# Kernel optimization log

Measured on AMD Instinct MI355X. Metric: run time of the kernel, lower is better.

The kernel has to match this reference:

```python
import jax, jax.numpy as jnp
import numpy as np

N, F, D, H = 8192, 128, 128, 2
LEAKY_ALPHA = 0.3  # keras.layers.LeakyReLU default


def setup_inputs() -> dict:
    key = jax.random.key(0)
    ks = jax.random.split(key, 8)
    x = jax.random.normal(ks[0], (N, F), dtype=jnp.float32)
    # sparse-ish binary adjacency with self loops, stored dense (as the module does)
    adj = (jax.random.uniform(ks[1], (N, N)) < 0.01).astype(jnp.float32)
    adj = jnp.clip(adj + jnp.eye(N, dtype=jnp.float32), 0.0, 1.0)
    s = 1.0 / np.sqrt(F)
    Wmap = jax.random.normal(ks[2], (H, F, D), dtype=jnp.float32) * s
    a1_w = jax.random.normal(ks[3], (H, D), dtype=jnp.float32) * (1.0 / np.sqrt(D))
    a2_w = jax.random.normal(ks[4], (H, D), dtype=jnp.float32) * (1.0 / np.sqrt(D))
    a1_b = jnp.zeros((H,), dtype=jnp.float32)
    a2_b = jnp.zeros((H,), dtype=jnp.float32)
    kernel = jax.random.normal(ks[5], (H, F, D), dtype=jnp.float32) * s
    bias = jnp.zeros((H, N, D), dtype=jnp.float32)
    return {"x": x, "adj": adj, "Wmap": Wmap, "a1_w": a1_w, "a1_b": a1_b,
            "a2_w": a2_w, "a2_b": a2_b, "kernel": kernel, "bias": bias}


def reference(x, adj, Wmap, a1_w, a1_b, a2_w, a2_b, kernel, bias):
    # per-head Conv1D(k=1, no bias): node-wise linear map  [H, N, D]
    mapped = jnp.einsum('nf,hfd->hnd', x, Wmap)
    # per-head Conv1D(k=1) scalar scores  [H, N]
    sa1 = jnp.einsum('hnd,hd->hn', mapped, a1_w) + a1_b[:, None]
    sa2 = jnp.einsum('hnd,hd->hn', mapped, a2_w) + a2_b[:, None]
    # additive score masked multiplicatively by adjacency:  [H, N, N]
    w = adj[None, :, :] * sa1[:, :, None] + adj[None, :, :] * sa2[:, None, :]
    w = jnp.where(w >= 0, w, LEAKY_ALPHA * w)
    att = jax.nn.softmax(w, axis=-1)  # softmax over neighbors (incl. zeroed entries, as in source)
    value = jnp.einsum('nf,hfd->hnd', x, kernel)
    out = jnp.einsum('hnm,hmd->hnd', att, value) + bias  # [H, N, D]
    return out.mean(axis=0)  # attn_heads_reduction='average', linear activation
```

## Files before the change

kernel.cpp:

```cpp
#include <hip/hip_runtime.h>

#define NN 8192
#define FF 128
#define DD 128
#define HH 2
#define ALPHA 0.3f
#define MAXNNZ 1024

typedef float v4f __attribute__((ext_vector_type(4)));

__global__ __launch_bounds__(256) void prep_kernel(
    const float* __restrict__ Wmap, const float* __restrict__ a1w,
    const float* __restrict__ a2w, const float* __restrict__ x,
    float* __restrict__ c1, float* __restrict__ c2, float* __restrict__ xsum) {
  int b = blockIdx.x;
  int t = threadIdx.x;
  if (b == 128) {
    int h = t >> 7, f = t & 127;
    const float* wrow = Wmap + ((size_t)h * FF + f) * DD;
    const float* a1 = a1w + h * DD;
    const float* a2 = a2w + h * DD;
    float s1 = 0.f, s2 = 0.f;
    #pragma unroll 8
    for (int d = 0; d < DD; d++) {
      float w = wrow[d];
      s1 += w * a1[d];
      s2 += w * a2[d];
    }
    c1[t] = s1;
    c2[t] = s2;
  } else {
    int f = t & 127, rh = t >> 7;
    const float* xp = x + ((size_t)(b * 64 + rh) * FF) + f;
    float s = 0.f;
    #pragma unroll 8
    for (int r = 0; r < 64; r += 2) s += xp[(size_t)r * FF];
    atomicAdd(&xsum[f], s);
  }
}

__global__ __launch_bounds__(128) void sa_kernel(
    const float* __restrict__ x, const float* __restrict__ c1,
    const float* __restrict__ c2, const float* __restrict__ a1b,
    const float* __restrict__ a2b, float* __restrict__ sa1, float* __restrict__ sa2) {
  int n = blockIdx.x;
  int f = threadIdx.x;
  float xv = x[(size_t)n * FF + f];
  float p00 = xv * c1[f];
  float p01 = xv * c1[FF + f];
  float p10 = xv * c2[f];
  float p11 = xv * c2[FF + f];
  #pragma unroll
  for (int o = 32; o > 0; o >>= 1) {
    p00 += __shfl_down(p00, o);
    p01 += __shfl_down(p01, o);
    p10 += __shfl_down(p10, o);
    p11 += __shfl_down(p11, o);
  }
  __shared__ float part[2][4];
  int w = f >> 6;
  if ((f & 63) == 0) {
    part[w][0] = p00; part[w][1] = p01; part[w][2] = p10; part[w][3] = p11;
  }
  __syncthreads();
  if (f == 0) {
    sa1[n]      = part[0][0] + part[1][0] + a1b[0];
    sa1[NN + n] = part[0][1] + part[1][1] + a1b[1];
    sa2[n]      = part[0][2] + part[1][2] + a2b[0];
    sa2[NN + n] = part[0][3] + part[1][3] + a2b[1];
  }
}

__global__ __launch_bounds__(128) void colsum_kernel(
    const float* __restrict__ xsum, const float* __restrict__ kern,
    float* __restrict__ colsum) {
  int h = blockIdx.x, d = threadIdx.x;
  const float* kb = kern + (size_t)h * FF * DD + d;
  float s = 0.f;
  #pragma unroll 8
  for (int f = 0; f < FF; f++) s += xsum[f] * kb[(size_t)f * DD];
  colsum[h * DD + d] = s;
}

__global__ __launch_bounds__(256) void gat_gather(
    const float* __restrict__ adj, const float* __restrict__ x,
    const float* __restrict__ sa1, const float* __restrict__ sa2,
    float* __restrict__ gs, float* __restrict__ cinv) {
  int i = blockIdx.x;
  __shared__ int idxbuf[MAXNNZ];
  __shared__ float em1buf[HH][MAXNNZ];
  __shared__ int cnt;
  __shared__ float wred[4][HH];
  __shared__ float sume_sh[HH];
  __shared__ float red2[HH][FF];
  int t = threadIdx.x;
  if (t == 0) cnt = 0;
  __syncthreads();

  const v4f* arow = (const v4f*)(adj + (size_t)i * NN);
  #pragma unroll
  for (int q = 0; q < 8; q++) {
    int f4 = q * 256 + t;
    v4f a = __builtin_nontemporal_load(&arow[f4]);
    int j0 = f4 * 4;
    if (a.x != 0.f) { int p = atomicAdd(&cnt, 1); if (p < MAXNNZ) idxbuf[p] = j0; }
    if (a.y != 0.f) { int p = atomicAdd(&cnt, 1); if (p < MAXNNZ) idxbuf[p] = j0 + 1; }
    if (a.z != 0.f) { int p = atomicAdd(&cnt, 1); if (p < MAXNNZ) idxbuf[p] = j0 + 2; }
    if (a.w != 0.f) { int p = atomicAdd(&cnt, 1); if (p < MAXNNZ) idxbuf[p] = j0 + 3; }
  }
  __syncthreads();
  int count = min(cnt, MAXNNZ);

  float s10 = sa1[i];
  float s11 = sa1[NN + i];
  float l0 = 0.f, l1 = 0.f;
  for (int k = t; k < count; k += 256) {
    int j = idxbuf[k];
    float w0 = s10 + sa2[j];
    float w1 = s11 + sa2[NN + j];
    w0 = (w0 >= 0.f) ? w0 : ALPHA * w0;
    w1 = (w1 >= 0.f) ? w1 : ALPHA * w1;
    float e0 = __expf(w0) - 1.f;
    float e1 = __expf(w1) - 1.f;
    em1buf[0][k] = e0;
    em1buf[1][k] = e1;
    l0 += e0;
    l1 += e1;
  }
  #pragma unroll
  for (int o = 32; o > 0; o >>= 1) {
    l0 += __shfl_down(l0, o);
    l1 += __shfl_down(l1, o);
  }
  int wid = t >> 6;
  if ((t & 63) == 0) { wred[wid][0] = l0; wred[wid][1] = l1; }
  __syncthreads();
  if (t == 0) {
    sume_sh[0] = wred[0][0] + wred[1][0] + wred[2][0] + wred[3][0];
    sume_sh[1] = wred[0][1] + wred[1][1] + wred[2][1] + wred[3][1];
  }
  __syncthreads();

  int ks = t >> 7, f = t & 127;
  float a0 = 0.f, a1 = 0.f;
  const float* xb = x + f;
  #pragma unroll 4
  for (int k = ks; k < count; k += 2) {
    int j = idxbuf[k];
    float xv = xb[(size_t)j * FF];
    a0 += em1buf[0][k] * xv;
    a1 += em1buf[1][k] * xv;
  }
  if (ks == 1) { red2[0][f] = a0; red2[1][f] = a1; }
  __syncthreads();
  if (ks == 0) {
    float inv0 = 0.5f / ((float)NN + sume_sh[0]);
    float inv1 = 0.5f / ((float)NN + sume_sh[1]);
    float g0 = (a0 + red2[0][f]) * inv0;
    float g1 = (a1 + red2[1][f]) * inv1;
    gs[(size_t)i * (HH * FF) + f]      = g0;
    gs[(size_t)i * (HH * FF) + FF + f] = g1;
    if (f == 0) { cinv[i] = inv0; cinv[NN + i] = inv1; }
  }
}

__global__ __launch_bounds__(256) void out_gemm(
    const float* __restrict__ gs, const float* __restrict__ kern,
    const float* __restrict__ cinv, const float* __restrict__ colsum,
    const float* __restrict__ bias, float* __restrict__ out) {
  int row0 = blockIdx.x * 32;
  __shared__ float Bl[64 * 128];
  __shared__ float Al[32 * 129];
  const float4* Bg4 = (const float4*)kern;
  const float4* Ag4 = (const float4*)(gs + (size_t)row0 * 256);
  float4* Bl4 = (float4*)Bl;
  int tid = threadIdx.x;
  int cg = tid & 31;
  int rg = tid >> 5;
  float4 acc[4];
  #pragma unroll
  for (int m = 0; m < 4; m++) acc[m] = make_float4(0.f, 0.f, 0.f, 0.f);

  for (int ka = 0; ka < 2; ka++) {
    __syncthreads();
    #pragma unroll
    for (int q = 0; q < 4; q++) {
      int idx = q * 256 + tid;
      int r = idx >> 5, c4 = idx & 31;
      float4 g = Ag4[r * 64 + ka * 32 + c4];
      Al[r * 129 + c4 * 4 + 0] = g.x;
      Al[r * 129 + c4 * 4 + 1] = g.y;
      Al[r * 129 + c4 * 4 + 2] = g.z;
      Al[r * 129 + c4 * 4 + 3] = g.w;
    }
    #pragma unroll
    for (int kpi = 0; kpi < 2; kpi++) {
      int kp = ka * 2 + kpi;
      __syncthreads();
      #pragma unroll
      for (int q = 0; q < 8; q++)
        Bl4[q * 256 + tid] = Bg4[kp * 2048 + q * 256 + tid];
      __syncthreads();
      for (int k2 = 0; k2 < 64; k2++) {
        float4 bv = *(const float4*)&Bl[k2 * 128 + cg * 4];
        #pragma unroll
        for (int m = 0; m < 4; m++) {
          float av = Al[(rg + m * 8) * 129 + kpi * 64 + k2];
          acc[m].x += av * bv.x;
          acc[m].y += av * bv.y;
          acc[m].z += av * bv.z;
          acc[m].w += av * bv.w;
        }
      }
    }
  }

  float4 cs0 = *(const float4*)&colsum[cg * 4];
  float4 cs1 = *(const float4*)&colsum[DD + cg * 4];
  #pragma unroll
  for (int m = 0; m < 4; m++) {
    int r = row0 + rg + m * 8;
    float ci0 = cinv[r];
    float ci1 = cinv[NN + r];
    float4 b0 = *(const float4*)&bias[((size_t)0 * NN + r) * DD + cg * 4];
    float4 b1 = *(const float4*)&bias[((size_t)1 * NN + r) * DD + cg * 4];
    float4 o;
    o.x = acc[m].x + ci0 * cs0.x + ci1 * cs1.x + 0.5f * (b0.x + b1.x);
    o.y = acc[m].y + ci0 * cs0.y + ci1 * cs1.y + 0.5f * (b0.y + b1.y);
    o.z = acc[m].z + ci0 * cs0.z + ci1 * cs1.z + 0.5f * (b0.z + b1.z);
    o.w = acc[m].w + ci0 * cs0.w + ci1 * cs1.w + 0.5f * (b0.w + b1.w);
    *(float4*)&out[(size_t)r * DD + cg * 4] = o;
  }
}

extern "C" void kernel_launch(void* const* d_in, const int* in_sizes, int n_in,
                              void* d_out, int out_size, void* d_ws, size_t ws_size,
                              hipStream_t stream) {
  const float* x    = (const float*)d_in[0];
  const float* adj  = (const float*)d_in[1];
  const float* Wmap = (const float*)d_in[2];
  const float* a1w  = (const float*)d_in[3];
  const float* a1b  = (const float*)d_in[4];
  const float* a2w  = (const float*)d_in[5];
  const float* a2b  = (const float*)d_in[6];
  const float* kern = (const float*)d_in[7];
  const float* bias = (const float*)d_in[8];
  float* out = (float*)d_out;
  float* ws  = (float*)d_ws;

  float* c1     = ws;
  float* c2     = ws + 256;
  float* sa1    = ws + 512;
  float* sa2    = ws + 16896;
  float* xsum   = ws + 33280;
  float* colsum = ws + 33408;
  float* cinv   = ws + 33664;
  float* gs     = ws + 50048;

  hipMemsetAsync(xsum, 0, FF * sizeof(float), stream);
  prep_kernel<<<129, 256, 0, stream>>>(Wmap, a1w, a2w, x, c1, c2, xsum);
  sa_kernel<<<NN, 128, 0, stream>>>(x, c1, c2, a1b, a2b, sa1, sa2);
  colsum_kernel<<<HH, 128, 0, stream>>>(xsum, kern, colsum);
  gat_gather<<<NN, 256, 0, stream>>>(adj, x, sa1, sa2, gs, cinv);
  out_gemm<<<NN / 32, 256, 0, stream>>>(gs, kern, cinv, colsum, bias, out);
}
```

Before: 428.6 us.

## Split adjacency scan from edge gather and fold colsum term into GEMM input

Splits the fused gather kernel into an adjacency scan that writes per-row neighbor index lists and a separate edge-gather kernel that vectorizes feature loads across 8 edge groups. The constant softmax term is folded in by adding xsum into the gathered row before the GEMM, removing the colsum kernel and the cinv epilogue. sa2 is packed as float2, and the GEMM uses float4 LDS reads with padded rows. This adds global traffic for the index lists and an extra launch.

```diff
diff --git a/kernel.cpp b/kernel.cpp
--- a/kernel.cpp
+++ b/kernel.cpp
@@ -42,7 +42,7 @@
 __global__ __launch_bounds__(128) void sa_kernel(
     const float* __restrict__ x, const float* __restrict__ c1,
     const float* __restrict__ c2, const float* __restrict__ a1b,
-    const float* __restrict__ a2b, float* __restrict__ sa1, float* __restrict__ sa2) {
+    const float* __restrict__ a2b, float* __restrict__ sa1, float* __restrict__ sa2p) {
   int n = blockIdx.x;
   int f = threadIdx.x;
   float xv = x[(size_t)n * FF + f];
@@ -66,37 +66,20 @@
   if (f == 0) {
     sa1[n]      = part[0][0] + part[1][0] + a1b[0];
     sa1[NN + n] = part[0][1] + part[1][1] + a1b[1];
-    sa2[n]      = part[0][2] + part[1][2] + a2b[0];
-    sa2[NN + n] = part[0][3] + part[1][3] + a2b[1];
-  }
-}
-
-__global__ __launch_bounds__(128) void colsum_kernel(
-    const float* __restrict__ xsum, const float* __restrict__ kern,
-    float* __restrict__ colsum) {
-  int h = blockIdx.x, d = threadIdx.x;
-  const float* kb = kern + (size_t)h * FF * DD + d;
-  float s = 0.f;
-  #pragma unroll 8
-  for (int f = 0; f < FF; f++) s += xsum[f] * kb[(size_t)f * DD];
-  colsum[h * DD + d] = s;
-}
-
-__global__ __launch_bounds__(256) void gat_gather(
-    const float* __restrict__ adj, const float* __restrict__ x,
-    const float* __restrict__ sa1, const float* __restrict__ sa2,
-    float* __restrict__ gs, float* __restrict__ cinv) {
+    ((float2*)sa2p)[n] = make_float2(part[0][2] + part[1][2] + a2b[0],
+                                     part[0][3] + part[1][3] + a2b[1]);
+  }
+}
+
+__global__ __launch_bounds__(256) void adj_scan(
+    const float* __restrict__ adj, int* __restrict__ counts,
+    int* __restrict__ idxw) {
   int i = blockIdx.x;
   __shared__ int idxbuf[MAXNNZ];
-  __shared__ float em1buf[HH][MAXNNZ];
   __shared__ int cnt;
-  __shared__ float wred[4][HH];
-  __shared__ float sume_sh[HH];
-  __shared__ float red2[HH][FF];
   int t = threadIdx.x;
   if (t == 0) cnt = 0;
   __syncthreads();
-
   const v4f* arow = (const v4f*)(adj + (size_t)i * NN);
   #pragma unroll
   for (int q = 0; q < 8; q++) {
@@ -110,14 +93,36 @@
   }
   __syncthreads();
   int count = min(cnt, MAXNNZ);
+  if (t == 0) counts[i] = count;
+  int* dst = idxw + (size_t)i * MAXNNZ;
+  for (int k = t; k < count; k += 256) dst[k] = idxbuf[k];
+}
+
+__global__ __launch_bounds__(256) void edge_gather(
+    const int* __restrict__ counts, const int* __restrict__ idxw,
+    const float* __restrict__ x, const float* __restrict__ sa1,
+    const float* __restrict__ sa2p, const float* __restrict__ xsum,
+    float* __restrict__ gs) {
+  int i = blockIdx.x;
+  __shared__ int idxbuf[MAXNNZ];
+  __shared__ float em1buf[HH][MAXNNZ];
+  __shared__ float wred[4][HH];
+  __shared__ float sume_sh[HH];
+  __shared__ v4f vred[HH][8][32];
+  int t = threadIdx.x;
+  int count = counts[i];
+  const int* src = idxw + (size_t)i * MAXNNZ;
+  for (int k = t; k < count; k += 256) idxbuf[k] = src[k];
+  __syncthreads();
 
   float s10 = sa1[i];
   float s11 = sa1[NN + i];
   float l0 = 0.f, l1 = 0.f;
   for (int k = t; k < count; k += 256) {
     int j = idxbuf[k];
-    float w0 = s10 + sa2[j];
-    float w1 = s11 + sa2[NN + j];
+    float2 s2 = ((const float2*)sa2p)[j];
+    float w0 = s10 + s2.x;
+    float w1 = s11 + s2.y;
     w0 = (w0 >= 0.f) ? w0 : ALPHA * w0;
     w1 = (w1 >= 0.f) ? w1 : ALPHA * w1;
     float e0 = __expf(w0) - 1.f;
@@ -141,45 +146,47 @@
   }
   __syncthreads();
 
-  int ks = t >> 7, f = t & 127;
-  float a0 = 0.f, a1 = 0.f;
-  const float* xb = x + f;
+  int sub = t & 31;
+  int eg  = t >> 5;
+  v4f acc0 = {0.f, 0.f, 0.f, 0.f}, acc1 = {0.f, 0.f, 0.f, 0.f};
+  const v4f* xb = (const v4f*)x;
   #pragma unroll 4
-  for (int k = ks; k < count; k += 2) {
+  for (int k = eg; k < count; k += 8) {
     int j = idxbuf[k];
-    float xv = xb[(size_t)j * FF];
-    a0 += em1buf[0][k] * xv;
-    a1 += em1buf[1][k] * xv;
-  }
-  if (ks == 1) { red2[0][f] = a0; red2[1][f] = a1; }
-  __syncthreads();
-  if (ks == 0) {
-    float inv0 = 0.5f / ((float)NN + sume_sh[0]);
-    float inv1 = 0.5f / ((float)NN + sume_sh[1]);
-    float g0 = (a0 + red2[0][f]) * inv0;
-    float g1 = (a1 + red2[1][f]) * inv1;
-    gs[(size_t)i * (HH * FF) + f]      = g0;
-    gs[(size_t)i * (HH * FF) + FF + f] = g1;
-    if (f == 0) { cinv[i] = inv0; cinv[NN + i] = inv1; }
+    v4f xv = xb[(size_t)j * 32 + sub];
+    acc0 += em1buf[0][k] * xv;
+    acc1 += em1buf[1][k] * xv;
+  }
+  vred[0][eg][sub] = acc0;
+  vred[1][eg][sub] = acc1;
+  __syncthreads();
+  if (t < 64) {
+    int h = t >> 5, s = t & 31;
+    v4f v = vred[h][0][s];
+    #pragma unroll
+    for (int e = 1; e < 8; e++) v += vred[h][e][s];
+    float inv = 0.5f / ((float)NN + sume_sh[h]);
+    v4f xs = ((const v4f*)xsum)[s];
+    v4f g = (v + xs) * inv;
+    ((v4f*)(gs + (size_t)i * (HH * FF)))[h * 32 + s] = g;
   }
 }
 
 __global__ __launch_bounds__(256) void out_gemm(
     const float* __restrict__ gs, const float* __restrict__ kern,
-    const float* __restrict__ cinv, const float* __restrict__ colsum,
     const float* __restrict__ bias, float* __restrict__ out) {
   int row0 = blockIdx.x * 32;
   __shared__ float Bl[64 * 128];
-  __shared__ float Al[32 * 129];
+  __shared__ float Al[32 * 132];
   const float4* Bg4 = (const float4*)kern;
   const float4* Ag4 = (const float4*)(gs + (size_t)row0 * 256);
   float4* Bl4 = (float4*)Bl;
   int tid = threadIdx.x;
   int cg = tid & 31;
   int rg = tid >> 5;
-  float4 acc[4];
-  #pragma unroll
-  for (int m = 0; m < 4; m++) acc[m] = make_float4(0.f, 0.f, 0.f, 0.f);
+  v4f acc[4];
+  #pragma unroll
+  for (int m = 0; m < 4; m++) acc[m] = (v4f){0.f, 0.f, 0.f, 0.f};
 
   for (int ka = 0; ka < 2; ka++) {
     __syncthreads();
@@ -188,10 +195,7 @@
       int idx = q * 256 + tid;
       int r = idx >> 5, c4 = idx & 31;
       float4 g = Ag4[r * 64 + ka * 32 + c4];
-      Al[r * 129 + c4 * 4 + 0] = g.x;
-      Al[r * 129 + c4 * 4 + 1] = g.y;
-      Al[r * 129 + c4 * 4 + 2] = g.z;
-      Al[r * 129 + c4 * 4 + 3] = g.w;
+      *(float4*)&Al[r * 132 + c4 * 4] = g;
     }
     #pragma unroll
     for (int kpi = 0; kpi < 2; kpi++) {
@@ -201,35 +205,31 @@
       for (int q = 0; q < 8; q++)
         Bl4[q * 256 + tid] = Bg4[kp * 2048 + q * 256 + tid];
       __syncthreads();
-      for (int k2 = 0; k2 < 64; k2++) {
-        float4 bv = *(const float4*)&Bl[k2 * 128 + cg * 4];
+      #pragma unroll 4
+      for (int kg = 0; kg < 16; kg++) {
+        v4f bv0 = *(const v4f*)&Bl[(kg * 4 + 0) * 128 + cg * 4];
+        v4f bv1 = *(const v4f*)&Bl[(kg * 4 + 1) * 128 + cg * 4];
+        v4f bv2 = *(const v4f*)&Bl[(kg * 4 + 2) * 128 + cg * 4];
+        v4f bv3 = *(const v4f*)&Bl[(kg * 4 + 3) * 128 + cg * 4];
         #pragma unroll
         for (int m = 0; m < 4; m++) {
-          float av = Al[(rg + m * 8) * 129 + kpi * 64 + k2];
-          acc[m].x += av * bv.x;
-          acc[m].y += av * bv.y;
-          acc[m].z += av * bv.z;
-          acc[m].w += av * bv.w;
+          v4f a4 = *(const v4f*)&Al[(rg + m * 8) * 132 + kpi * 64 + kg * 4];
+          acc[m] += a4.x * bv0;
+          acc[m] += a4.y * bv1;
+          acc[m] += a4.z * bv2;
+          acc[m] += a4.w * bv3;
         }
       }
     }
   }
 
-  float4 cs0 = *(const float4*)&colsum[cg * 4];
-  float4 cs1 = *(const float4*)&colsum[DD + cg * 4];
   #pragma unroll
   for (int m = 0; m < 4; m++) {
     int r = row0 + rg + m * 8;
-    float ci0 = cinv[r];
-    float ci1 = cinv[NN + r];
-    float4 b0 = *(const float4*)&bias[((size_t)0 * NN + r) * DD + cg * 4];
-    float4 b1 = *(const float4*)&bias[((size_t)1 * NN + r) * DD + cg * 4];
-    float4 o;
-    o.x = acc[m].x + ci0 * cs0.x + ci1 * cs1.x + 0.5f * (b0.x + b1.x);
-    o.y = acc[m].y + ci0 * cs0.y + ci1 * cs1.y + 0.5f * (b0.y + b1.y);
-    o.z = acc[m].z + ci0 * cs0.z + ci1 * cs1.z + 0.5f * (b0.z + b1.z);
-    o.w = acc[m].w + ci0 * cs0.w + ci1 * cs1.w + 0.5f * (b0.w + b1.w);
-    *(float4*)&out[(size_t)r * DD + cg * 4] = o;
+    v4f b0 = *(const v4f*)&bias[((size_t)0 * NN + r) * DD + cg * 4];
+    v4f b1 = *(const v4f*)&bias[((size_t)1 * NN + r) * DD + cg * 4];
+    v4f o = acc[m] + 0.5f * (b0 + b1);
+    *(v4f*)&out[(size_t)r * DD + cg * 4] = o;
   }
 }
 
@@ -248,19 +248,19 @@
   float* out = (float*)d_out;
   float* ws  = (float*)d_ws;
 
-  float* c1     = ws;
-  float* c2     = ws + 256;
-  float* sa1    = ws + 512;
-  float* sa2    = ws + 16896;
-  float* xsum   = ws + 33280;
-  float* colsum = ws + 33408;
-  float* cinv   = ws + 33664;
-  float* gs     = ws + 50048;
+  float* c1   = ws;
+  float* c2   = ws + 256;
+  float* sa1  = ws + 512;
+  float* sa2p = ws + 16896;
+  float* xsum = ws + 33280;
+  float* gs   = ws + 33408;
+  int*   counts = (int*)(ws + 2130560);
+  int*   idxw   = (int*)(ws + 2138752);
 
   hipMemsetAsync(xsum, 0, FF * sizeof(float), stream);
   prep_kernel<<<129, 256, 0, stream>>>(Wmap, a1w, a2w, x, c1, c2, xsum);
-  sa_kernel<<<NN, 128, 0, stream>>>(x, c1, c2, a1b, a2b, sa1, sa2);
-  colsum_kernel<<<HH, 128, 0, stream>>>(xsum, kern, colsum);
-  gat_gather<<<NN, 256, 0, stream>>>(adj, x, sa1, sa2, gs, cinv);
-  out_gemm<<<NN / 32, 256, 0, stream>>>(gs, kern, cinv, colsum, bias, out);
-}
+  sa_kernel<<<NN, 128, 0, stream>>>(x, c1, c2, a1b, a2b, sa1, sa2p);
+  adj_scan<<<NN, 256, 0, stream>>>(adj, counts, idxw);
+  edge_gather<<<NN, 256, 0, stream>>>(counts, idxw, x, sa1, sa2p, xsum, gs);
+  out_gemm<<<NN / 32, 256, 0, stream>>>(gs, kern, bias, out);
+}
```

Measured after the change: 418.5 us. -2.3%, faster.
